# Optimization experiments

Hardware: AMD Instinct MI355X
Metric: run time of the kernel (lower is better)

## Reference

```python
import jax, jax.numpy as jnp
import numpy as np

B, N, T = 512, 24, 25
IN, L, H, OUT = 8, 64, 256, 128


def quat_mul(q, r):
    w1, x1, y1, z1 = jnp.split(q, 4, -1)
    w2, x2, y2, z2 = jnp.split(r, 4, -1)
    return jnp.concatenate([
        w1 * w2 - x1 * x2 - y1 * y2 - z1 * z2,
        w1 * x2 + x1 * w2 + y1 * z2 - z1 * y2,
        w1 * y2 - x1 * z2 + y1 * w2 + z1 * x2,
        w1 * z2 + x1 * y2 - y1 * x2 + z1 * w2], -1)


def node_linear(x, W, b, G):
    # per-node weights [N,F,O], then graph-influence mixing G[N,N]
    y = jnp.einsum('bnf,nfo->bno', x, W) + b
    return jnp.einsum('mn,bno->bmo', G, y)


def graph_linear(x, W, b, G):
    # shared weights [F,O], then graph-influence mixing
    y = jnp.einsum('bnf,fo->bno', x, W) + b
    return jnp.einsum('mn,bno->bmo', G, y)


def lstm_step(x, h, c, Wx, Wh, b, G):
    gates = jnp.einsum('bnf,nfo->bno', x, Wx) + jnp.einsum('bnf,nfo->bno', h, Wh) + b
    gates = jnp.einsum('mn,bno->bmo', G, gates)
    i, f, g, o = jnp.split(gates, 4, -1)
    c = jax.nn.sigmoid(f) * c + jax.nn.sigmoid(i) * jnp.tanh(g)
    h = jax.nn.sigmoid(o) * jnp.tanh(c)
    return h, c


def _p(key, shape, scale):
    return jax.random.normal(key, shape, jnp.float32) * scale


def setup_inputs() -> dict:
    key = jax.random.key(0)
    ks = jax.random.split(key, 20)
    in0 = L + IN
    inp = {
        'x': jax.random.normal(ks[0], (B, 1, N, IN), jnp.float32),
        'enc': jax.random.normal(ks[1], (B, 1, N, H), jnp.float32),
        'z': jax.random.normal(ks[2], (B, 1, N, L), jnp.float32),
        'y': jax.random.normal(ks[3], (B, T, N, 4), jnp.float32),
        'G': jnp.eye(N, dtype=jnp.float32) + 0.02 * jax.random.normal(ks[4], (N, N), jnp.float32),
        'Wx0': _p(ks[5], (N, in0, 4 * OUT), in0 ** -0.5),
        'Wh0': _p(ks[6], (N, OUT, 4 * OUT), OUT ** -0.5),
        'b0': jnp.zeros((N, 4 * OUT), jnp.float32),
        'Wx1': _p(ks[7], (N, OUT, 4 * OUT), OUT ** -0.5),
        'Wh1': _p(ks[8], (N, OUT, 4 * OUT), OUT ** -0.5),
        'b1': jnp.zeros((N, 4 * OUT), jnp.float32),
        'fc_W': _p(ks[9], (N, OUT, OUT), OUT ** -0.5),
        'fc_b': jnp.zeros((N, OUT), jnp.float32),
        'fc2_W': _p(ks[10], (N, OUT, OUT), OUT ** -0.5),
        'fc2_b': jnp.zeros((N, OUT), jnp.float32),
        'ih1_W': _p(ks[11], (H, OUT), H ** -0.5),
        'ih1_b': jnp.zeros((OUT,), jnp.float32),
        'ih2_W': _p(ks[12], (H, OUT), H ** -0.5),
        'ih2_b': jnp.zeros((OUT,), jnp.float32),
        'loc_W': _p(ks[13], (OUT, 3), OUT ** -0.5),
        'loc_b': jnp.zeros((3,), jnp.float32),
        'logz_W': _p(ks[14], (OUT, 4), OUT ** -0.5),
        'logz_b': jnp.zeros((4,), jnp.float32),
    }
    return inp


def reference(x, enc, z, y, G, Wx0, Wh0, b0, Wx1, Wh1, b1, fc_W, fc_b, fc2_W, fc2_b,
              ih1_W, ih1_b, ih2_W, ih2_b, loc_W, loc_b, logz_W, logz_b):
    # eval mode: dropout = identity, no teacher forcing (y unused); rnn2/xi2 are dead code.
    xs, zs, encs = x[:, 0], z[:, 0], enc[:, 0]          # [B,N,*]
    h0 = graph_linear(encs, ih1_W, ih1_b, G)            # shared initial h for both layers
    c0 = graph_linear(encs, ih2_W, ih2_b, G)            # shared initial c for both layers
    loc_start0 = xs[..., :4]
    xi0 = jnp.concatenate([zs, xs], -1)                 # [B,N,L+IN]

    def step(carry, _):
        xi, loc_start, h1, c1, h2, c2 = carry
        h1, c1 = lstm_step(xi, h1, c1, Wx0, Wh0, b0, G)
        h2, c2 = lstm_step(h1, h2, c2, Wx1, Wh1, b1, G)
        yi = jnp.tanh(h2)
        yi1 = jnp.tanh(node_linear(yi, fc_W, fc_b, G))
        yi2 = jnp.tanh(node_linear(yi, fc2_W, fc2_b, G))
        loc3 = graph_linear(yi1, loc_W, loc_b, G)       # [B,N,3]
        log_Z = graph_linear(yi2, logz_W, logz_b, G)    # [B,N,4]
        w = jnp.ones(loc3.shape[:-1] + (1,), loc3.dtype)
        loc4 = jnp.concatenate([w, loc3], -1)
        loc_d = loc4 * jax.lax.rsqrt(jnp.sum(loc4 * loc4, -1, keepdims=True))  # validate
        loc = quat_mul(loc_start, loc_d)                # state_representation.sum
        xi_next = jnp.concatenate([zs, loc, loc_d], -1)
        return (xi_next, loc, h1, c1, h2, c2), (loc, log_Z)

    _, (locs, logzs) = jax.lax.scan(step, (xi0, loc_start0, h0, c0, h0, c0), None, length=T)
    out = jnp.moveaxis(locs, 0, 1)[:, :, None]          # [B,T,1,N,4]
    out_log_diag = jnp.moveaxis(logzs, 0, 1)[:, :, None]
    return out, out_log_diag
```

## Files before the change

### kernel.cpp

```cpp
#include <hip/hip_runtime.h>
#include <math.h>

#define Bsz 512
#define Nn  24
#define Tt  25

typedef _Float16 f16;
typedef _Float16 f16x8 __attribute__((ext_vector_type(8)));
typedef _Float16 f16x4 __attribute__((ext_vector_type(4)));
typedef float f32x4 __attribute__((ext_vector_type(4)));

template <int FM, int FN>
__global__ __launch_bounds__(256) void gemm_mfma(
    const f16* __restrict__ Act, const float* __restrict__ Act32, int Ka,
    const f16* __restrict__ W, size_t wstride,
    const float* __restrict__ bias, int bstride,
    const f16* __restrict__ base16,
    f16* __restrict__ Y, int O)
{
    const int BM = FM * 32, BN = FN * 32;
    const int n  = blockIdx.z;
    const int o0 = blockIdx.x * BM;
    const int b0 = blockIdx.y * BN;
    const int tid  = threadIdx.x;
    const int wave = tid >> 6, lane = tid & 63;
    const int wm = (wave >> 1) * FM * 16;
    const int wn = (wave & 1) * FN * 16;
    const int m16 = lane & 15, quad = lane >> 4;

    __shared__ __attribute__((aligned(16))) f16 sW[BM][72];
    __shared__ __attribute__((aligned(16))) f16 sB[BN][72];

    const f16* Wn = W + (size_t)n * wstride;
    f32x4 acc[FM][FN] = {};

    const int r  = tid >> 3;
    const int cc = (tid & 7) * 8;

    for (int k0 = 0; k0 < Ka; k0 += 64) {
        for (int row = r; row < BM; row += 32)
            *(f16x8*)&sW[row][cc] = *(const f16x8*)&Wn[(size_t)(o0 + row) * Ka + k0 + cc];
        if (Act) {
            for (int row = r; row < BN; row += 32)
                *(f16x8*)&sB[row][cc] = *(const f16x8*)&Act[((size_t)(b0 + row) * Nn + n) * Ka + k0 + cc];
        } else {
            for (int row = r; row < BN; row += 32) {
                const float* src = &Act32[((size_t)(b0 + row) * Nn + n) * Ka + k0 + cc];
                f16x8 v;
#pragma unroll
                for (int u = 0; u < 8; u++) v[u] = (f16)src[u];
                *(f16x8*)&sB[row][cc] = v;
            }
        }
        __syncthreads();
#pragma unroll
        for (int kk = 0; kk < 64; kk += 32) {
            f16x8 af[FM], bf[FN];
#pragma unroll
            for (int i = 0; i < FM; i++)
                af[i] = *(const f16x8*)&sW[wm + i * 16 + m16][kk + quad * 8];
#pragma unroll
            for (int j = 0; j < FN; j++)
                bf[j] = *(const f16x8*)&sB[wn + j * 16 + m16][kk + quad * 8];
#pragma unroll
            for (int i = 0; i < FM; i++)
#pragma unroll
                for (int j = 0; j < FN; j++)
                    acc[i][j] = __builtin_amdgcn_mfma_f32_16x16x32_f16(af[i], bf[j], acc[i][j], 0, 0, 0);
        }
        __syncthreads();
    }
#pragma unroll
    for (int i = 0; i < FM; i++) {
        const int orow = o0 + wm + i * 16 + quad * 4;
        float4 bv = make_float4(0.f, 0.f, 0.f, 0.f);
        if (bias) bv = *(const float4*)&bias[(size_t)n * bstride + orow];
#pragma unroll
        for (int j = 0; j < FN; j++) {
            const int bcol = b0 + wn + j * 16 + m16;
            size_t yi = ((size_t)bcol * Nn + n) * (size_t)O + orow;
            float v0 = acc[i][j][0] + bv.x;
            float v1 = acc[i][j][1] + bv.y;
            float v2 = acc[i][j][2] + bv.z;
            float v3 = acc[i][j][3] + bv.w;
            if (base16) {
                f16x4 bb = *(const f16x4*)&base16[yi];
                v0 += (float)bb[0]; v1 += (float)bb[1];
                v2 += (float)bb[2]; v3 += (float)bb[3];
            }
            f16x4 o4; o4[0] = (f16)v0; o4[1] = (f16)v1; o4[2] = (f16)v2; o4[3] = (f16)v3;
            *(f16x4*)&Y[yi] = o4;
        }
    }
}

__global__ __launch_bounds__(256) void prep_w01(
    const float* __restrict__ Wx0, const float* __restrict__ Wh0,
    const float* __restrict__ Wx1, const float* __restrict__ Wh1,
    f16* __restrict__ Wz, f16* __restrict__ Wt0, f16* __restrict__ Wt1)
{
    size_t idx = (size_t)blockIdx.x * 256 + threadIdx.x;
    const size_t nz = (size_t)Nn * 512 * 64;
    const size_t n0 = (size_t)Nn * 512 * 192;
    const size_t n1 = (size_t)Nn * 512 * 256;
    if (idx < nz) {
        int k = idx & 63; int o = (idx >> 6) & 511; int n = (int)(idx >> 15);
        Wz[idx] = (f16)Wx0[((size_t)n * 72 + k) * 512 + o];
    } else if (idx < nz + n0) {
        size_t i2 = idx - nz;
        int k = (int)(i2 % 192);
        size_t no = i2 / 192;
        int o = (int)(no & 511); int n = (int)(no >> 9);
        float v = 0.f;
        if (k < 8) v = Wx0[((size_t)n * 72 + 64 + k) * 512 + o];
        else if (k < 136) v = Wh0[((size_t)n * 128 + (k - 8)) * 512 + o];
        Wt0[i2] = (f16)v;
    } else if (idx < nz + n0 + n1) {
        size_t i3 = idx - nz - n0;
        int k = (int)(i3 & 255);
        size_t no = i3 >> 8;
        int o = (int)(no & 511); int n = (int)(no >> 9);
        float v = (k < 128) ? Wx1[((size_t)n * 128 + k) * 512 + o]
                            : Wh1[((size_t)n * 128 + (k - 128)) * 512 + o];
        Wt1[i3] = (f16)v;
    }
}

__global__ __launch_bounds__(256) void prep_wf(
    const float* __restrict__ fcW, const float* __restrict__ fc2W,
    f16* __restrict__ Wtf)
{
    size_t idx = (size_t)blockIdx.x * 256 + threadIdx.x;
    if (idx >= (size_t)Nn * 256 * 128) return;
    int k = (int)(idx & 127);
    size_t no = idx >> 7;
    int o = (int)(no & 255); int n = (int)(no >> 8);
    float v = (o < 128) ? fcW[((size_t)n * 128 + k) * 128 + o]
                        : fc2W[((size_t)n * 128 + k) * 128 + (o - 128)];
    Wtf[idx] = (f16)v;
}

__global__ __launch_bounds__(256) void prep_wi(
    const float* __restrict__ ih1W, const float* __restrict__ ih2W,
    const float* __restrict__ ih1b, const float* __restrict__ ih2b,
    const float* __restrict__ fcb, const float* __restrict__ fc2b,
    f16* __restrict__ Wti, float* __restrict__ bi, float* __restrict__ bcat)
{
    int idx = blockIdx.x * 256 + threadIdx.x;
    int k = idx & 255, o = idx >> 8;
    Wti[idx] = (f16)((o < 128) ? ih1W[(size_t)k * 128 + o] : ih2W[(size_t)k * 128 + (o - 128)]);
    if (idx < 256) bi[idx] = (idx < 128) ? ih1b[idx] : ih2b[idx - 128];
    if (idx < Nn * 256) {
        int n = idx >> 8, oo = idx & 255;
        bcat[idx] = (oo < 128) ? fcb[n * 128 + oo] : fc2b[n * 128 + (oo - 128)];
    }
}

__global__ __launch_bounds__(256) void init_xi(
    const float* __restrict__ x, f16* __restrict__ xi2, float* __restrict__ ls)
{
    size_t idx = (size_t)blockIdx.x * 256 + threadIdx.x;
    const size_t total = (size_t)Bsz * Nn * 192;
    if (idx < total) {
        size_t bn = idx / 192;
        int k = (int)(idx - bn * 192);
        if (k < 8) xi2[idx] = (f16)x[bn * 8 + k];
        else if (k >= 136) xi2[idx] = (f16)0.f;
    }
    if (idx < (size_t)Bsz * Nn * 4) {
        size_t bn = idx >> 2;
        ls[idx] = x[bn * 8 + (idx & 3)];
    }
}

__global__ __launch_bounds__(256) void mix_init(
    const f16* __restrict__ Yhc, const float* __restrict__ G,
    f16* __restrict__ xi2, f16* __restrict__ l2cat,
    float* __restrict__ c1, float* __restrict__ c2)
{
    const int b = blockIdx.x;
    const int tid = threadIdx.x;
    __shared__ float sY[6144], sG[576];
    for (int i = tid; i < 576; i += 256) sG[i] = G[i];
    for (int v = tid; v < 768; v += 256) {
        int c8 = (v & 31) * 8, n = v >> 5;
        f16x8 t = *(const f16x8*)&Yhc[((size_t)b * Nn + n) * 256 + c8];
        float* d = &sY[n * 256 + c8];
#pragma unroll
        for (int u = 0; u < 8; u++) d[u] = (float)t[u];
    }
    __syncthreads();
    for (int w = tid; w < 3072; w += 256) {
        int o = w & 127, m = w >> 7;
        float ah = 0.f, ac = 0.f;
#pragma unroll
        for (int n = 0; n < 24; n++) {
            float g = sG[m * 24 + n];
            ah += g * sY[n * 256 + o];
            ac += g * sY[n * 256 + 128 + o];
        }
        size_t row = (size_t)b * Nn + m;
        f16 hf = (f16)ah;
        xi2[row * 192 + 8 + o] = hf;
        l2cat[row * 256 + o] = hf;
        l2cat[row * 256 + 128 + o] = hf;
        c1[row * 128 + o] = ac;
        c2[row * 128 + o] = ac;
    }
}

__global__ __launch_bounds__(256) void mixlstm(
    const f16* __restrict__ Ypre, const float* __restrict__ G,
    float* __restrict__ c,
    f16* __restrict__ dstA, int strideA,
    f16* __restrict__ dstB, int strideB, int tanhB)
{
    const int b = blockIdx.x;
    const int jt = blockIdx.y * 64;
    const int tid = threadIdx.x;
    __shared__ float sY[6144];
    __shared__ float sG[576];
    for (int i = tid; i < 576; i += 256) sG[i] = G[i];
    for (int v = tid; v < 768; v += 256) {
        int j8 = (v & 7) * 8, g = (v >> 3) & 3, n = v >> 5;
        f16x8 t = *(const f16x8*)&Ypre[((size_t)b * Nn + n) * 512 + g * 128 + jt + j8];
        float* d = &sY[n * 256 + g * 64 + j8];
#pragma unroll
        for (int u = 0; u < 8; u++) d[u] = (float)t[u];
    }
    __syncthreads();
    for (int w = tid; w < 1536; w += 256) {
        int j = w & 63, m = w >> 6;
        float gi = 0.f, gf = 0.f, gg = 0.f, go = 0.f;
        const float* gr = &sG[m * 24];
#pragma unroll
        for (int n = 0; n < 24; n++) {
            float g = gr[n];
            gi += g * sY[n * 256 + j];
            gf += g * sY[n * 256 + 64 + j];
            gg += g * sY[n * 256 + 128 + j];
            go += g * sY[n * 256 + 192 + j];
        }
        int col = jt + j;
        size_t row = (size_t)b * Nn + m;
        float cv = c[row * 128 + col];
        float si = 1.f / (1.f + expf(-gi));
        float sf = 1.f / (1.f + expf(-gf));
        float so = 1.f / (1.f + expf(-go));
        float tg = tanhf(gg);
        cv = sf * cv + si * tg;
        c[row * 128 + col] = cv;
        float h = so * tanhf(cv);
        dstA[row * strideA + col] = (f16)h;
        dstB[row * strideB + col] = (f16)(tanhB ? tanhf(h) : h);
    }
}

__global__ __launch_bounds__(256) void finstep(
    const f16* __restrict__ p, const float* __restrict__ G,
    const float* __restrict__ locW, const float* __restrict__ locb,
    const float* __restrict__ lzW, const float* __restrict__ lzb,
    float* __restrict__ ls, f16* __restrict__ xi2,
    float* __restrict__ out, int t)
{
    const int b = blockIdx.x;
    const int tid = threadIdx.x;
    __shared__ float sP[6144], sY1[3072], sY2[3072];
    __shared__ float sG[576];
    __shared__ float sLp[24][3], sZp[24][4], sL3[24][3], sZ3[24][4];
    for (int i = tid; i < 576; i += 256) sG[i] = G[i];
    for (int v = tid; v < 768; v += 256) {
        int c8 = (v & 31) * 8, n = v >> 5;
        f16x8 tv = *(const f16x8*)&p[((size_t)b * Nn + n) * 256 + c8];
        float* d = &sP[n * 256 + c8];
#pragma unroll
        for (int u = 0; u < 8; u++) d[u] = (float)tv[u];
    }
    __syncthreads();
    for (int w = tid; w < 3072; w += 256) {
        int o = w & 127, m = w >> 7;
        float a1 = 0.f, a2 = 0.f;
#pragma unroll
        for (int n = 0; n < 24; n++) {
            float g = sG[m * 24 + n];
            a1 += g * sP[n * 256 + o];
            a2 += g * sP[n * 256 + 128 + o];
        }
        sY1[w] = tanhf(a1);
        sY2[w] = tanhf(a2);
    }
    __syncthreads();
    if (tid < 72) {
        int m = tid / 3, j = tid - m * 3;
        float s = locb[j];
        for (int o = 0; o < 128; o++) s += sY1[m * 128 + o] * locW[o * 3 + j];
        sLp[m][j] = s;
    } else if (tid < 168) {
        int w2 = tid - 72; int m = w2 >> 2, j = w2 & 3;
        float s = lzb[j];
        for (int o = 0; o < 128; o++) s += sY2[m * 128 + o] * lzW[o * 4 + j];
        sZp[m][j] = s;
    }
    __syncthreads();
    if (tid < 72) {
        int m = tid / 3, j = tid - m * 3;
        float s = 0.f;
#pragma unroll
        for (int n = 0; n < 24; n++) s += sG[m * 24 + n] * sLp[n][j];
        sL3[m][j] = s;
    } else if (tid < 168) {
        int w2 = tid - 72; int m = w2 >> 2, j = w2 & 3;
        float s = 0.f;
#pragma unroll
        for (int n = 0; n < 24; n++) s += sG[m * 24 + n] * sZp[n][j];
        sZ3[m][j] = s;
    }
    __syncthreads();
    if (tid < 24) {
        int m = tid;
        float xx = sL3[m][0], xy = sL3[m][1], xz = sL3[m][2];
        float r = rsqrtf(1.f + xx * xx + xy * xy + xz * xz);
        float dw = r, dx = xx * r, dy = xy * r, dz = xz * r;
        size_t li = ((size_t)b * Nn + m) * 4;
        float qw = ls[li], qx = ls[li + 1], qy = ls[li + 2], qz = ls[li + 3];
        float lw = qw * dw - qx * dx - qy * dy - qz * dz;
        float lx = qw * dx + qx * dw + qy * dz - qz * dy;
        float ly = qw * dy - qx * dz + qy * dw + qz * dx;
        float lz = qw * dz + qx * dy - qy * dx + qz * dw;
        size_t oi = (((size_t)b * Tt + t) * Nn + m) * 4;
        out[oi + 0] = lw; out[oi + 1] = lx; out[oi + 2] = ly; out[oi + 3] = lz;
        size_t zi = (size_t)Bsz * Tt * Nn * 4 + oi;
        out[zi + 0] = sZ3[m][0]; out[zi + 1] = sZ3[m][1];
        out[zi + 2] = sZ3[m][2]; out[zi + 3] = sZ3[m][3];
        ls[li] = lw; ls[li + 1] = lx; ls[li + 2] = ly; ls[li + 3] = lz;
        size_t xb = ((size_t)b * Nn + m) * 192;
        xi2[xb + 0] = (f16)lw; xi2[xb + 1] = (f16)lx; xi2[xb + 2] = (f16)ly; xi2[xb + 3] = (f16)lz;
        xi2[xb + 4] = (f16)dw; xi2[xb + 5] = (f16)dx; xi2[xb + 6] = (f16)dy; xi2[xb + 7] = (f16)dz;
    }
}

extern "C" void kernel_launch(void* const* d_in, const int* in_sizes, int n_in,
                              void* d_out, int out_size, void* d_ws, size_t ws_size,
                              hipStream_t stream)
{
    const float* x    = (const float*)d_in[0];
    const float* enc  = (const float*)d_in[1];
    const float* z    = (const float*)d_in[2];
    const float* G    = (const float*)d_in[4];
    const float* Wx0  = (const float*)d_in[5];
    const float* Wh0  = (const float*)d_in[6];
    const float* b0i  = (const float*)d_in[7];
    const float* Wx1  = (const float*)d_in[8];
    const float* Wh1  = (const float*)d_in[9];
    const float* b1i  = (const float*)d_in[10];
    const float* fcW  = (const float*)d_in[11];
    const float* fcb  = (const float*)d_in[12];
    const float* fc2W = (const float*)d_in[13];
    const float* fc2b = (const float*)d_in[14];
    const float* ih1W = (const float*)d_in[15];
    const float* ih1b = (const float*)d_in[16];
    const float* ih2W = (const float*)d_in[17];
    const float* ih2b = (const float*)d_in[18];
    const float* locW = (const float*)d_in[19];
    const float* locb = (const float*)d_in[20];
    const float* lzW  = (const float*)d_in[21];
    const float* lzb  = (const float*)d_in[22];
    float* out = (float*)d_out;

    const size_t BN = (size_t)Bsz * Nn;
    char* wp = (char*)d_ws;
    size_t off = 0;
    auto carve = [&](size_t bytes) -> char* {
        char* pc = wp + off;
        off += (bytes + 255) & ~(size_t)255;
        return pc;
    };
    f16*   Wz     = (f16*)carve((size_t)Nn * 512 * 64 * 2);
    f16*   Wt0    = (f16*)carve((size_t)Nn * 512 * 192 * 2);
    f16*   Wt1    = (f16*)carve((size_t)Nn * 512 * 256 * 2);
    f16*   Wtf    = (f16*)carve((size_t)Nn * 256 * 128 * 2);
    f16*   Wti    = (f16*)carve((size_t)256 * 256 * 2);
    float* bcat   = (float*)carve((size_t)Nn * 256 * 4);
    float* bi     = (float*)carve(256 * 4);
    f16*   base1  = (f16*)carve(BN * 512 * 2);
    f16*   xi2    = (f16*)carve(BN * 192 * 2);
    f16*   l2cat  = (f16*)carve(BN * 256 * 2);
    f16*   yib    = (f16*)carve(BN * 128 * 2);
    float* c1     = (float*)carve(BN * 128 * 4);
    float* c2     = (float*)carve(BN * 128 * 4);
    float* ls     = (float*)carve(BN * 4 * 4);
    f16*   yp     = (f16*)carve(BN * 512 * 2);
    f16*   pbuf   = (f16*)carve(BN * 256 * 2);

    prep_w01<<<24576, 256, 0, stream>>>(Wx0, Wh0, Wx1, Wh1, Wz, Wt0, Wt1);
    prep_wf<<<3072, 256, 0, stream>>>(fcW, fc2W, Wtf);
    prep_wi<<<256, 256, 0, stream>>>(ih1W, ih2W, ih1b, ih2b, fcb, fc2b, Wti, bi, bcat);
    init_xi<<<9216, 256, 0, stream>>>(x, xi2, ls);

    gemm_mfma<2, 4><<<dim3(8, 4, 24), 256, 0, stream>>>(
        nullptr, z, 64, Wz, (size_t)512 * 64, b0i, 512, nullptr, base1, 512);
    gemm_mfma<2, 4><<<dim3(4, 4, 24), 256, 0, stream>>>(
        nullptr, enc, 256, Wti, 0, bi, 0, nullptr, yp, 256);
    mix_init<<<512, 256, 0, stream>>>(yp, G, xi2, l2cat, c1, c2);

    for (int t = 0; t < Tt; t++) {
        gemm_mfma<2, 4><<<dim3(8, 4, 24), 256, 0, stream>>>(
            xi2, nullptr, 192, Wt0, (size_t)512 * 192, nullptr, 0, base1, yp, 512);
        mixlstm<<<dim3(512, 2), 256, 0, stream>>>(yp, G, c1, xi2 + 8, 192, l2cat, 256, 0);
        gemm_mfma<2, 4><<<dim3(8, 4, 24), 256, 0, stream>>>(
            l2cat, nullptr, 256, Wt1, (size_t)512 * 256, b1i, 512, nullptr, yp, 512);
        mixlstm<<<dim3(512, 2), 256, 0, stream>>>(yp, G, c2, l2cat + 128, 256, yib, 128, 1);
        gemm_mfma<2, 4><<<dim3(4, 4, 24), 256, 0, stream>>>(
            yib, nullptr, 128, Wtf, (size_t)256 * 128, bcat, 256, nullptr, pbuf, 256);
        finstep<<<512, 256, 0, stream>>>(pbuf, G, locW, locb, lzW, lzb, ls, xi2, out, t);
    }
}
```

Measured before the change: 2.502 ms.

## Fuse per-timestep kernel chain into one persistent cooperative kernel with grid syncs

The 150 per-timestep kernel launches (GEMMs, LSTM mixing, final step) are replaced by a single cooperative persistent kernel that loops over time and phases, with grid-wide syncs between phases. Blocks stride over virtual tiles in place of per-launch grids. This removes launch overhead and inter-kernel gaps. In exchange the grid is capped at 512 blocks and pays the cost of grid barriers, and shared memory is reused across phases.

Result: slower. 8.413 ms (+236.3%).

```diff
diff --git a/kernel.cpp b/kernel.cpp
--- a/kernel.cpp
+++ b/kernel.cpp
@@ -1,5 +1,8 @@
 #include <hip/hip_runtime.h>
+#include <hip/hip_cooperative_groups.h>
 #include <math.h>
+
+namespace cg = cooperative_groups;
 
 #define Bsz 512
 #define Nn  24
@@ -209,133 +212,265 @@
     }
 }
 
-__global__ __launch_bounds__(256) void mixlstm(
-    const f16* __restrict__ Ypre, const float* __restrict__ G,
-    float* __restrict__ c,
+struct StepArgs {
+    const float* G;
+    const f16* Wt0; const f16* Wt1; const f16* Wtf;
+    const float* b1i; const float* bcat;
+    const f16* base1;
+    f16* xi2; f16* l2cat; f16* yib; f16* yp; f16* pbuf;
+    float* c1; float* c2; float* ls;
+    const float* locW; const float* locb; const float* lzW; const float* lzb;
+    float* out;
+};
+
+#define SMEM_BYTES 50688
+
+template <int FM, int FN>
+__device__ __forceinline__ void gemm_phase(
+    char* smraw,
+    const f16* __restrict__ Act, int Ka,
+    const f16* __restrict__ W, size_t wstride,
+    const float* __restrict__ bias, int bstride,
+    const f16* __restrict__ base16,
+    f16* __restrict__ Y, int O,
+    int ntx, int nty, int gridb, int bid, int tid)
+{
+    const int BM = FM * 32, BN = FN * 32;
+    f16 (*sW)[72] = (f16 (*)[72])smraw;
+    f16 (*sB)[72] = (f16 (*)[72])(smraw + (size_t)BM * 72 * 2);
+    const int wave = tid >> 6, lane = tid & 63;
+    const int wm = (wave >> 1) * FM * 16;
+    const int wn = (wave & 1) * FN * 16;
+    const int m16 = lane & 15, quad = lane >> 4;
+    const int r  = tid >> 3;
+    const int cc = (tid & 7) * 8;
+    const int nvt = ntx * nty * Nn;
+
+    for (int vt = bid; vt < nvt; vt += gridb) {
+        const int n   = vt / (ntx * nty);
+        const int rem = vt - n * ntx * nty;
+        const int o0  = (rem % ntx) * BM;
+        const int b0  = (rem / ntx) * BN;
+        const f16* Wn = W + (size_t)n * wstride;
+        f32x4 acc[FM][FN] = {};
+
+        for (int k0 = 0; k0 < Ka; k0 += 64) {
+            for (int row = r; row < BM; row += 32)
+                *(f16x8*)&sW[row][cc] = *(const f16x8*)&Wn[(size_t)(o0 + row) * Ka + k0 + cc];
+            for (int row = r; row < BN; row += 32)
+                *(f16x8*)&sB[row][cc] = *(const f16x8*)&Act[((size_t)(b0 + row) * Nn + n) * Ka + k0 + cc];
+            __syncthreads();
+#pragma unroll
+            for (int kk = 0; kk < 64; kk += 32) {
+                f16x8 af[FM], bf[FN];
+#pragma unroll
+                for (int i = 0; i < FM; i++)
+                    af[i] = *(const f16x8*)&sW[wm + i * 16 + m16][kk + quad * 8];
+#pragma unroll
+                for (int j = 0; j < FN; j++)
+                    bf[j] = *(const f16x8*)&sB[wn + j * 16 + m16][kk + quad * 8];
+#pragma unroll
+                for (int i = 0; i < FM; i++)
+#pragma unroll
+                    for (int j = 0; j < FN; j++)
+                        acc[i][j] = __builtin_amdgcn_mfma_f32_16x16x32_f16(af[i], bf[j], acc[i][j], 0, 0, 0);
+            }
+            __syncthreads();
+        }
+#pragma unroll
+        for (int i = 0; i < FM; i++) {
+            const int orow = o0 + wm + i * 16 + quad * 4;
+            float4 bv = make_float4(0.f, 0.f, 0.f, 0.f);
+            if (bias) bv = *(const float4*)&bias[(size_t)n * bstride + orow];
+#pragma unroll
+            for (int j = 0; j < FN; j++) {
+                const int bcol = b0 + wn + j * 16 + m16;
+                size_t yi = ((size_t)bcol * Nn + n) * (size_t)O + orow;
+                float v0 = acc[i][j][0] + bv.x;
+                float v1 = acc[i][j][1] + bv.y;
+                float v2 = acc[i][j][2] + bv.z;
+                float v3 = acc[i][j][3] + bv.w;
+                if (base16) {
+                    f16x4 bb = *(const f16x4*)&base16[yi];
+                    v0 += (float)bb[0]; v1 += (float)bb[1];
+                    v2 += (float)bb[2]; v3 += (float)bb[3];
+                }
+                f16x4 o4; o4[0] = (f16)v0; o4[1] = (f16)v1; o4[2] = (f16)v2; o4[3] = (f16)v3;
+                *(f16x4*)&Y[yi] = o4;
+            }
+        }
+    }
+}
+
+__device__ __forceinline__ void mixlstm_phase(
+    char* smraw, const float* sG,
+    const f16* __restrict__ Ypre, float* __restrict__ c,
     f16* __restrict__ dstA, int strideA,
-    f16* __restrict__ dstB, int strideB, int tanhB)
-{
-    const int b = blockIdx.x;
-    const int jt = blockIdx.y * 64;
-    const int tid = threadIdx.x;
-    __shared__ float sY[6144];
-    __shared__ float sG[576];
-    for (int i = tid; i < 576; i += 256) sG[i] = G[i];
-    for (int v = tid; v < 768; v += 256) {
-        int j8 = (v & 7) * 8, g = (v >> 3) & 3, n = v >> 5;
-        f16x8 t = *(const f16x8*)&Ypre[((size_t)b * Nn + n) * 512 + g * 128 + jt + j8];
-        float* d = &sY[n * 256 + g * 64 + j8];
-#pragma unroll
-        for (int u = 0; u < 8; u++) d[u] = (float)t[u];
-    }
-    __syncthreads();
-    for (int w = tid; w < 1536; w += 256) {
-        int j = w & 63, m = w >> 6;
-        float gi = 0.f, gf = 0.f, gg = 0.f, go = 0.f;
-        const float* gr = &sG[m * 24];
-#pragma unroll
-        for (int n = 0; n < 24; n++) {
-            float g = gr[n];
-            gi += g * sY[n * 256 + j];
-            gf += g * sY[n * 256 + 64 + j];
-            gg += g * sY[n * 256 + 128 + j];
-            go += g * sY[n * 256 + 192 + j];
-        }
-        int col = jt + j;
-        size_t row = (size_t)b * Nn + m;
-        float cv = c[row * 128 + col];
-        float si = 1.f / (1.f + expf(-gi));
-        float sf = 1.f / (1.f + expf(-gf));
-        float so = 1.f / (1.f + expf(-go));
-        float tg = tanhf(gg);
-        cv = sf * cv + si * tg;
-        c[row * 128 + col] = cv;
-        float h = so * tanhf(cv);
-        dstA[row * strideA + col] = (f16)h;
-        dstB[row * strideB + col] = (f16)(tanhB ? tanhf(h) : h);
-    }
-}
-
-__global__ __launch_bounds__(256) void finstep(
-    const f16* __restrict__ p, const float* __restrict__ G,
+    f16* __restrict__ dstB, int strideB, int tanhB,
+    int gridb, int bid, int tid)
+{
+    float* sY = (float*)smraw;
+    for (int vt = bid; vt < 1024; vt += gridb) {
+        const int b  = vt & 511;
+        const int jt = (vt >> 9) * 64;
+        for (int v = tid; v < 768; v += 256) {
+            int j8 = (v & 7) * 8, g = (v >> 3) & 3, n = v >> 5;
+            f16x8 t = *(const f16x8*)&Ypre[((size_t)b * Nn + n) * 512 + g * 128 + jt + j8];
+            float* d = &sY[n * 256 + g * 64 + j8];
+#pragma unroll
+            for (int u = 0; u < 8; u++) d[u] = (float)t[u];
+        }
+        __syncthreads();
+        for (int w = tid; w < 1536; w += 256) {
+            int j = w & 63, m = w >> 6;
+            float gi = 0.f, gf = 0.f, gg = 0.f, go = 0.f;
+            const float* gr = &sG[m * 24];
+#pragma unroll
+            for (int n = 0; n < 24; n++) {
+                float g = gr[n];
+                gi += g * sY[n * 256 + j];
+                gf += g * sY[n * 256 + 64 + j];
+                gg += g * sY[n * 256 + 128 + j];
+                go += g * sY[n * 256 + 192 + j];
+            }
+            int col = jt + j;
+            size_t row = (size_t)b * Nn + m;
+            float cv = c[row * 128 + col];
+            float si = 1.f / (1.f + expf(-gi));
+            float sf = 1.f / (1.f + expf(-gf));
+            float so = 1.f / (1.f + expf(-go));
+            float tg = tanhf(gg);
+            cv = sf * cv + si * tg;
+            c[row * 128 + col] = cv;
+            float h = so * tanhf(cv);
+            dstA[row * strideA + col] = (f16)h;
+            dstB[row * strideB + col] = (f16)(tanhB ? tanhf(h) : h);
+        }
+        __syncthreads();
+    }
+}
+
+__device__ __forceinline__ void finstep_phase(
+    char* smraw, const float* sG,
+    const f16* __restrict__ p,
     const float* __restrict__ locW, const float* __restrict__ locb,
     const float* __restrict__ lzW, const float* __restrict__ lzb,
     float* __restrict__ ls, f16* __restrict__ xi2,
-    float* __restrict__ out, int t)
-{
-    const int b = blockIdx.x;
-    const int tid = threadIdx.x;
-    __shared__ float sP[6144], sY1[3072], sY2[3072];
+    float* __restrict__ out, int t,
+    int gridb, int bid, int tid)
+{
+    float* sP  = (float*)smraw;
+    float* sY1 = (float*)(smraw + 24576);
+    float* sY2 = (float*)(smraw + 36864);
+    float (*sLp)[3] = (float (*)[3])(smraw + 49152);
+    float (*sZp)[4] = (float (*)[4])(smraw + 49440);
+    float (*sL3)[3] = (float (*)[3])(smraw + 49824);
+    float (*sZ3)[4] = (float (*)[4])(smraw + 50112);
+
+    for (int b = bid; b < Bsz; b += gridb) {
+        for (int v = tid; v < 768; v += 256) {
+            int c8 = (v & 31) * 8, n = v >> 5;
+            f16x8 tv = *(const f16x8*)&p[((size_t)b * Nn + n) * 256 + c8];
+            float* d = &sP[n * 256 + c8];
+#pragma unroll
+            for (int u = 0; u < 8; u++) d[u] = (float)tv[u];
+        }
+        __syncthreads();
+        for (int w = tid; w < 3072; w += 256) {
+            int o = w & 127, m = w >> 7;
+            float a1 = 0.f, a2 = 0.f;
+#pragma unroll
+            for (int n = 0; n < 24; n++) {
+                float g = sG[m * 24 + n];
+                a1 += g * sP[n * 256 + o];
+                a2 += g * sP[n * 256 + 128 + o];
+            }
+            sY1[w] = tanhf(a1);
+            sY2[w] = tanhf(a2);
+        }
+        __syncthreads();
+        if (tid < 72) {
+            int m = tid / 3, j = tid - m * 3;
+            float s = locb[j];
+            for (int o = 0; o < 128; o++) s += sY1[m * 128 + o] * locW[o * 3 + j];
+            sLp[m][j] = s;
+        } else if (tid < 168) {
+            int w2 = tid - 72; int m = w2 >> 2, j = w2 & 3;
+            float s = lzb[j];
+            for (int o = 0; o < 128; o++) s += sY2[m * 128 + o] * lzW[o * 4 + j];
+            sZp[m][j] = s;
+        }
+        __syncthreads();
+        if (tid < 72) {
+            int m = tid / 3, j = tid - m * 3;
+            float s = 0.f;
+#pragma unroll
+            for (int n = 0; n < 24; n++) s += sG[m * 24 + n] * sLp[n][j];
+            sL3[m][j] = s;
+        } else if (tid < 168) {
+            int w2 = tid - 72; int m = w2 >> 2, j = w2 & 3;
+            float s = 0.f;
+#pragma unroll
+            for (int n = 0; n < 24; n++) s += sG[m * 24 + n] * sZp[n][j];
+            sZ3[m][j] = s;
+        }
+        __syncthreads();
+        if (tid < 24) {
+            int m = tid;
+            float xx = sL3[m][0], xy = sL3[m][1], xz = sL3[m][2];
+            float r = rsqrtf(1.f + xx * xx + xy * xy + xz * xz);
+            float dw = r, dx = xx * r, dy = xy * r, dz = xz * r;
+            size_t li = ((size_t)b * Nn + m) * 4;
+            float qw = ls[li], qx = ls[li + 1], qy = ls[li + 2], qz = ls[li + 3];
+            float lw = qw * dw - qx * dx - qy * dy - qz * dz;
+            float lx = qw * dx + qx * dw + qy * dz - qz * dy;
+            float ly = qw * dy - qx * dz + qy * dw + qz * dx;
+            float lz = qw * dz + qx * dy - qy * dx + qz * dw;
+            size_t oi = (((size_t)b * Tt + t) * Nn + m) * 4;
+            out[oi + 0] = lw; out[oi + 1] = lx; out[oi + 2] = ly; out[oi + 3] = lz;
+            size_t zi = (size_t)Bsz * Tt * Nn * 4 + oi;
+            out[zi + 0] = sZ3[m][0]; out[zi + 1] = sZ3[m][1];
+            out[zi + 2] = sZ3[m][2]; out[zi + 3] = sZ3[m][3];
+            ls[li] = lw; ls[li + 1] = lx; ls[li + 2] = ly; ls[li + 3] = lz;
+            size_t xb = ((size_t)b * Nn + m) * 192;
+            xi2[xb + 0] = (f16)lw; xi2[xb + 1] = (f16)lx; xi2[xb + 2] = (f16)ly; xi2[xb + 3] = (f16)lz;
+            xi2[xb + 4] = (f16)dw; xi2[xb + 5] = (f16)dx; xi2[xb + 6] = (f16)dy; xi2[xb + 7] = (f16)dz;
+        }
+        __syncthreads();
+    }
+}
+
+__global__ __launch_bounds__(256, 2) void step_loop(StepArgs a)
+{
     __shared__ float sG[576];
-    __shared__ float sLp[24][3], sZp[24][4], sL3[24][3], sZ3[24][4];
-    for (int i = tid; i < 576; i += 256) sG[i] = G[i];
-    for (int v = tid; v < 768; v += 256) {
-        int c8 = (v & 31) * 8, n = v >> 5;
-        f16x8 tv = *(const f16x8*)&p[((size_t)b * Nn + n) * 256 + c8];
-        float* d = &sP[n * 256 + c8];
-#pragma unroll
-        for (int u = 0; u < 8; u++) d[u] = (float)tv[u];
-    }
-    __syncthreads();
-    for (int w = tid; w < 3072; w += 256) {
-        int o = w & 127, m = w >> 7;
-        float a1 = 0.f, a2 = 0.f;
-#pragma unroll
-        for (int n = 0; n < 24; n++) {
-            float g = sG[m * 24 + n];
-            a1 += g * sP[n * 256 + o];
-            a2 += g * sP[n * 256 + 128 + o];
-        }
-        sY1[w] = tanhf(a1);
-        sY2[w] = tanhf(a2);
-    }
-    __syncthreads();
-    if (tid < 72) {
-        int m = tid / 3, j = tid - m * 3;
-        float s = locb[j];
-        for (int o = 0; o < 128; o++) s += sY1[m * 128 + o] * locW[o * 3 + j];
-        sLp[m][j] = s;
-    } else if (tid < 168) {
-        int w2 = tid - 72; int m = w2 >> 2, j = w2 & 3;
-        float s = lzb[j];
-        for (int o = 0; o < 128; o++) s += sY2[m * 128 + o] * lzW[o * 4 + j];
-        sZp[m][j] = s;
-    }
-    __syncthreads();
-    if (tid < 72) {
-        int m = tid / 3, j = tid - m * 3;
-        float s = 0.f;
-#pragma unroll
-        for (int n = 0; n < 24; n++) s += sG[m * 24 + n] * sLp[n][j];
-        sL3[m][j] = s;
-    } else if (tid < 168) {
-        int w2 = tid - 72; int m = w2 >> 2, j = w2 & 3;
-        float s = 0.f;
-#pragma unroll
-        for (int n = 0; n < 24; n++) s += sG[m * 24 + n] * sZp[n][j];
-        sZ3[m][j] = s;
-    }
-    __syncthreads();
-    if (tid < 24) {
-        int m = tid;
-        float xx = sL3[m][0], xy = sL3[m][1], xz = sL3[m][2];
-        float r = rsqrtf(1.f + xx * xx + xy * xy + xz * xz);
-        float dw = r, dx = xx * r, dy = xy * r, dz = xz * r;
-        size_t li = ((size_t)b * Nn + m) * 4;
-        float qw = ls[li], qx = ls[li + 1], qy = ls[li + 2], qz = ls[li + 3];
-        float lw = qw * dw - qx * dx - qy * dy - qz * dz;
-        float lx = qw * dx + qx * dw + qy * dz - qz * dy;
-        float ly = qw * dy - qx * dz + qy * dw + qz * dx;
-        float lz = qw * dz + qx * dy - qy * dx + qz * dw;
-        size_t oi = (((size_t)b * Tt + t) * Nn + m) * 4;
-        out[oi + 0] = lw; out[oi + 1] = lx; out[oi + 2] = ly; out[oi + 3] = lz;
-        size_t zi = (size_t)Bsz * Tt * Nn * 4 + oi;
-        out[zi + 0] = sZ3[m][0]; out[zi + 1] = sZ3[m][1];
-        out[zi + 2] = sZ3[m][2]; out[zi + 3] = sZ3[m][3];
-        ls[li] = lw; ls[li + 1] = lx; ls[li + 2] = ly; ls[li + 3] = lz;
-        size_t xb = ((size_t)b * Nn + m) * 192;
-        xi2[xb + 0] = (f16)lw; xi2[xb + 1] = (f16)lx; xi2[xb + 2] = (f16)ly; xi2[xb + 3] = (f16)lz;
-        xi2[xb + 4] = (f16)dw; xi2[xb + 5] = (f16)dx; xi2[xb + 6] = (f16)dy; xi2[xb + 7] = (f16)dz;
+    __shared__ __attribute__((aligned(16))) char smem[SMEM_BYTES];
+
+    const int tid   = threadIdx.x;
+    const int bid   = blockIdx.x;
+    const int gridb = gridDim.x;
+    cg::grid_group gg = cg::this_grid();
+
+    for (int i = tid; i < 576; i += 256) sG[i] = a.G[i];
+
+    for (int t = 0; t < Tt; t++) {
+        gemm_phase<2, 4>(smem, a.xi2, 192, a.Wt0, (size_t)512 * 192,
+                         nullptr, 0, a.base1, a.yp, 512, 8, 4, gridb, bid, tid);
+        gg.sync();
+        mixlstm_phase(smem, sG, a.yp, a.c1, a.xi2 + 8, 192, a.l2cat, 256, 0,
+                      gridb, bid, tid);
+        gg.sync();
+        gemm_phase<2, 4>(smem, a.l2cat, 256, a.Wt1, (size_t)512 * 256,
+                         a.b1i, 512, nullptr, a.yp, 512, 8, 4, gridb, bid, tid);
+        gg.sync();
+        mixlstm_phase(smem, sG, a.yp, a.c2, a.l2cat + 128, 256, a.yib, 128, 1,
+                      gridb, bid, tid);
+        gg.sync();
+        gemm_phase<2, 4>(smem, a.yib, 128, a.Wtf, (size_t)256 * 128,
+                         a.bcat, 256, nullptr, a.pbuf, 256, 4, 4, gridb, bid, tid);
+        gg.sync();
+        finstep_phase(smem, sG, a.pbuf, a.locW, a.locb, a.lzW, a.lzb,
+                      a.ls, a.xi2, a.out, t, gridb, bid, tid);
+        gg.sync();
     }
 }
 
@@ -403,15 +538,21 @@
         nullptr, enc, 256, Wti, 0, bi, 0, nullptr, yp, 256);
     mix_init<<<512, 256, 0, stream>>>(yp, G, xi2, l2cat, c1, c2);
 
-    for (int t = 0; t < Tt; t++) {
-        gemm_mfma<2, 4><<<dim3(8, 4, 24), 256, 0, stream>>>(
-            xi2, nullptr, 192, Wt0, (size_t)512 * 192, nullptr, 0, base1, yp, 512);
-        mixlstm<<<dim3(512, 2), 256, 0, stream>>>(yp, G, c1, xi2 + 8, 192, l2cat, 256, 0);
-        gemm_mfma<2, 4><<<dim3(8, 4, 24), 256, 0, stream>>>(
-            l2cat, nullptr, 256, Wt1, (size_t)512 * 256, b1i, 512, nullptr, yp, 512);
-        mixlstm<<<dim3(512, 2), 256, 0, stream>>>(yp, G, c2, l2cat + 128, 256, yib, 128, 1);
-        gemm_mfma<2, 4><<<dim3(4, 4, 24), 256, 0, stream>>>(
-            yib, nullptr, 128, Wtf, (size_t)256 * 128, bcat, 256, nullptr, pbuf, 256);
-        finstep<<<512, 256, 0, stream>>>(pbuf, G, locW, locb, lzW, lzb, ls, xi2, out, t);
-    }
-}
+    StepArgs sa;
+    sa.G = G; sa.Wt0 = Wt0; sa.Wt1 = Wt1; sa.Wtf = Wtf;
+    sa.b1i = b1i; sa.bcat = bcat; sa.base1 = base1;
+    sa.xi2 = xi2; sa.l2cat = l2cat; sa.yib = yib; sa.yp = yp; sa.pbuf = pbuf;
+    sa.c1 = c1; sa.c2 = c2; sa.ls = ls;
+    sa.locW = locW; sa.locb = locb; sa.lzW = lzW; sa.lzb = lzb;
+    sa.out = out;
+
+    int maxb = 0;
+    if (hipOccupancyMaxActiveBlocksPerMultiprocessor(&maxb, step_loop, 256, 0) != hipSuccess || maxb < 1)
+        maxb = 1;
+    int nblk = maxb * 256;
+    if (nblk > 512) nblk = 512;
+
+    void* kargs[] = { (void*)&sa };
+    hipLaunchCooperativeKernel((const void*)step_loop, dim3(nblk), dim3(256),
+                               kargs, 0, stream);
+}
```
